# Kernel optimization log

Measured on AMD Instinct MI355X. Metric: run time of the kernel, lower is better.

The kernel has to match this reference:

```python
import jax, jax.numpy as jnp
import numpy as np

D_MODEL = 48
SSM_RATIO = 2
D_INNER = D_MODEL * SSM_RATIO   # 96
D_STATE = 16
DT_RANK = -(-D_MODEL // 16)     # ceil(48/16) = 3
K = 4                           # 4 scan directions
LAP_ITERS = 10
LAP_TAU = 0.1
B, DD, HH, WW = 2, 20, 20, 20   # L = 8000 (even)


def _lap_kernel(c):
    k = np.zeros((3, 3, 3), dtype=np.float32)
    k[1, 1, 1] = -6.0
    k[0, 1, 1] = k[2, 1, 1] = 1.0
    k[1, 0, 1] = k[1, 2, 1] = 1.0
    k[1, 1, 0] = k[1, 1, 2] = 1.0
    return jnp.asarray(np.tile(k[None, None], (c, 1, 1, 1, 1)))  # (C,1,3,3,3)


def _dwconv3d(x, w):
    # x: (B,C,D,H,W), w: (C,1,3,3,3) depthwise
    return jax.lax.conv_general_dilated(
        x, w, (1, 1, 1), 'SAME',
        dimension_numbers=('NCDHW', 'OIDHW', 'NCDHW'),
        feature_group_count=x.shape[1])


def _directions(feat):
    # feat: (B,C,D,H,W) -> (B,4,C,L): forward, flipped-L, channel-flipped, cross
    Bb, C, Dd, Hh, Ww = feat.shape
    L = Dd * Hh * Ww
    f = feat.reshape(Bb, C, L)
    bwd = f[:, :, ::-1]
    cb = feat[:, ::-1].reshape(Bb, C, L)
    half = (L + 1) // 2            # L is even here
    front = np.arange(half)
    back = np.arange(half, L)[::-1]
    cross_idx = np.stack([front, back], axis=1).reshape(-1)[:L]
    cross = f[:, :, cross_idx]
    return jnp.stack([f, bwd, cb, cross], axis=1)


def _selective_scan(u, delta, A, Bs, Cs, Ds):
    # u, delta: (b,k,d,l); A: (k,d,n); Bs, Cs: (b,k,n,l); Ds: (k,d)
    dl = jnp.moveaxis(delta, -1, 0)  # (l,b,k,d)
    ul = jnp.moveaxis(u, -1, 0)
    Bl = jnp.moveaxis(Bs, -1, 0)     # (l,b,k,n)
    Cl = jnp.moveaxis(Cs, -1, 0)
    h0 = jnp.zeros(u.shape[:3] + (A.shape[-1],), u.dtype)  # (b,k,d,n)

    def step(h, inp):
        d_t, u_t, b_t, c_t = inp
        dA = jnp.exp(d_t[..., None] * A[None])                    # (b,k,d,n)
        h = dA * h + (d_t * u_t)[..., None] * b_t[:, :, None, :]  # (b,k,d,n)
        y = jnp.einsum('bkdn,bkn->bkd', h, c_t)
        return h, y

    _, ys = jax.lax.scan(step, h0, (dl, ul, Bl, Cl))
    y = jnp.moveaxis(ys, 0, -1)  # (b,k,d,l)
    return y + Ds[None, :, :, None] * u


def setup_inputs() -> dict:
    key = jax.random.key(0)
    ks = jax.random.split(key, 10)

    def rn(k, shape, scale=0.02):
        return jax.random.normal(k, shape, dtype=jnp.float32) * scale

    x = jax.random.normal(ks[0], (B, DD, HH, WW, D_MODEL), dtype=jnp.float32)
    in_proj_w = rn(ks[1], (2 * D_INNER, D_MODEL))
    in_proj_cross_w = rn(ks[2], (D_INNER, D_MODEL))
    conv_w = rn(ks[3], (D_INNER, 1, 3, 3, 3), 0.1)
    conv_b = jnp.zeros((D_INNER,), jnp.float32)
    x_proj_weight = rn(ks[4], (K, DT_RANK + 2 * D_STATE, D_INNER))
    dt_std = DT_RANK ** -0.5
    dt_projs_weight = jax.random.uniform(ks[5], (K, D_INNER, DT_RANK), minval=-dt_std, maxval=dt_std, dtype=jnp.float32)
    dt = jnp.exp(jax.random.uniform(ks[6], (K, D_INNER)) * (np.log(0.1) - np.log(0.001)) + np.log(0.001))
    dt = jnp.clip(dt, 1e-4, None)
    dt_projs_bias = dt + jnp.log(-jnp.expm1(-dt))  # inverse softplus
    A_logs = jnp.log(jnp.tile(jnp.arange(1, D_STATE + 1, dtype=jnp.float32)[None], (K * D_INNER, 1)))
    Ds = jnp.ones((K * D_INNER,), jnp.float32)
    out_norm_w = jnp.ones((D_INNER,), jnp.float32)
    out_norm_b = jnp.zeros((D_INNER,), jnp.float32)
    out_proj_w = rn(ks[7], (D_MODEL, D_INNER))
    concat_w = rn(ks[8], (D_MODEL, 2 * D_MODEL))
    concat_b = jnp.zeros((D_MODEL,), jnp.float32)
    return dict(x=x, in_proj_w=in_proj_w, in_proj_cross_w=in_proj_cross_w,
                conv_w=conv_w, conv_b=conv_b, x_proj_weight=x_proj_weight,
                dt_projs_weight=dt_projs_weight, dt_projs_bias=dt_projs_bias,
                A_logs=A_logs, Ds=Ds, out_norm_w=out_norm_w, out_norm_b=out_norm_b,
                out_proj_w=out_proj_w, concat_w=concat_w, concat_b=concat_b)


def reference(x, in_proj_w, in_proj_cross_w, conv_w, conv_b, x_proj_weight,
              dt_projs_weight, dt_projs_bias, A_logs, Ds, out_norm_w,
              out_norm_b, out_proj_w, concat_w, concat_b):
    Bb, Dd, Hh, Ww, C = x.shape
    L = Dd * Hh * Ww
    xch = jnp.moveaxis(x, -1, 1)  # (B,C,D,H,W)

    # --- 3D Laplacian frequency decomposition: u_{k+1} = u_k + tau * lap(u_k)
    lap_k = _lap_kernel(C)
    u = xch
    for _ in range(LAP_ITERS):
        u = u + LAP_TAU * _dwconv3d(u, lap_k)
    low, high = u, xch - u
    cat = jnp.concatenate([low, high], axis=1)  # (B,2C,D,H,W)
    # 1x1x1 conv 2C -> C
    x_f = jnp.einsum('bcdhw,oc->bodhw', cat, concat_w) + concat_b[None, :, None, None, None]

    # --- CSS3D(x, x_f)
    xz = x @ in_proj_w.T                       # (B,D,H,W,2*d_inner)
    xi, z = jnp.split(xz, 2, axis=-1)
    xc = jnp.moveaxis(x_f, 1, -1) @ in_proj_cross_w.T  # (B,D,H,W,d_inner)
    xi = jnp.moveaxis(xi, -1, 1)               # (B,d_inner,D,H,W)
    xi = jax.nn.silu(_dwconv3d(xi, conv_w) + conv_b[None, :, None, None, None])
    xc = jnp.moveaxis(xc, -1, 1)

    xs = _directions(xi)    # (B,4,d_inner,L)
    xcs = _directions(xc)

    x_dbl = jnp.einsum('bkdl,kcd->bkcl', xcs, x_proj_weight)
    dts = x_dbl[:, :, :DT_RANK]
    Bs = x_dbl[:, :, DT_RANK:DT_RANK + D_STATE]
    Cs = x_dbl[:, :, DT_RANK + D_STATE:]
    dts = jnp.einsum('bkrl,kdr->bkdl', dts, dt_projs_weight)
    delta = jax.nn.softplus(dts + dt_projs_bias[None, :, :, None])
    A = -jnp.exp(A_logs.reshape(K, D_INNER, D_STATE))

    y = _selective_scan(xs, delta, A, Bs, Cs, Ds.reshape(K, D_INNER))
    y = y.mean(axis=1).reshape(Bb, D_INNER, Dd, Hh, Ww)
    y = jnp.moveaxis(y, 1, -1)                 # (B,D,H,W,d_inner)

    mu = y.mean(-1, keepdims=True)
    var = ((y - mu) ** 2).mean(-1, keepdims=True)
    y = (y - mu) / jnp.sqrt(var + 1e-5) * out_norm_w + out_norm_b

    y = y * jax.nn.sigmoid(z)
    return y @ out_proj_w.T                    # (B,D,H,W,d_model)
```

## Files before the change

kernel.cpp:

```cpp
#include <hip/hip_runtime.h>
#include <hip/hip_bf16.h>

typedef __hip_bfloat16 bf16;
typedef unsigned short u16;

#define L_  8000
#define CM  48
#define DI  96
#define DST 16
#define BB  2
#define NC  64
#define CS  125

#define W_IPW    0
#define W_IPCW   9216
#define W_CW     13824
#define W_CB     16416
#define W_XPW    16512
#define W_DTW    29952
#define W_DTB    31104
#define W_ALOG   31488
#define W_DSP    37632
#define W_NW     38016
#define W_NB     38112
#define W_OPW    38208
#define W_CCW    42816
#define W_CCB    47424
#define W_CVT_END 47472
#define W_WU     47472
#define W_WX     52080
#define W_BC     56688
#define W_ZT     56784
#define W_XIRAW  1592784
#define W_XT     3128784
#define W_UT     3896784
#define W_DTS    1592784
#define W_P      1784784
#define W_HLOC   2571216
#define W_HSTART 3357648
#define W_XIT    4664784
#define W_XCT    6200784
#define W_Y      4664784
#define W_F32_END 7736784
#define H_UP 0
#define H_BS 6144000
#define H_CS 7168000
#define H_END 8192000
#define NEED_BYTES ((size_t)W_F32_END*4 + (size_t)H_END*2)

__device__ __forceinline__ float b2f(bf16 v){ return __bfloat162float(v); }
__device__ __forceinline__ float bf2f(u16 v){ return __uint_as_float(((unsigned)v) << 16); }
__device__ __forceinline__ u16   f2b(float f){ bf16 h = __float2bfloat16(f); return *(u16*)&h; }
__device__ __forceinline__ float softplus(float tv){
    return fmaxf(tv, 0.f) + __logf(1.f + __expf(-fabsf(tv)));
}
template<int CTRL>
__device__ __forceinline__ float dppadd(float v){
    int x = __builtin_amdgcn_update_dpp(0, __float_as_int(v), CTRL, 0xF, 0xF, true);
    return v + __int_as_float(x);
}

__global__ __launch_bounds__(256) void k_xt(const void* __restrict__ xin,
                                            const u16* __restrict__ probe,
                                            float* __restrict__ xt){
    __shared__ float tileS[CM][65];
    int tile = blockIdx.x;
    int b = tile / 125, lt = (tile - b*125)*64;
    bool isb = (probe[0] != 0);
    for (int i = threadIdx.x; i < 64*CM; i += 256){
        int l = i / CM, c = i - (i/CM)*CM;
        size_t gi = ((size_t)b*L_ + lt + l)*CM + c;
        float v = isb ? b2f(((const bf16*)xin)[gi]) : ((const float*)xin)[gi];
        tileS[c][l] = v;
    }
    __syncthreads();
    for (int i = threadIdx.x; i < CM*64; i += 256){
        int c = i >> 6, l = i & 63;
        xt[((size_t)(b*CM + c))*L_ + lt + l] = tileS[c][l];
    }
}

struct CvtArgs { const void* src[15]; int beg[16]; };

__global__ __launch_bounds__(256) void k_cvt(CvtArgs a, float* __restrict__ dst){
    int i = blockIdx.x*256 + threadIdx.x;
    if (i >= W_CVT_END) return;
    bool isb = (((const u16*)a.src[9])[0] != 0);
    int s = 1;
    #pragma unroll
    for (int t = 2; t < 15; ++t) if (i >= a.beg[t]) s = t;
    int j = i - a.beg[s];
    dst[i] = isb ? b2f(((const bf16*)a.src[s])[j]) : ((const float*)a.src[s])[j];
}

__global__ __launch_bounds__(256) void k_zero_out(const u16* __restrict__ probe, void* out){
    int i = blockIdx.x*256 + threadIdx.x;
    if (i >= BB*L_*CM) return;
    if (probe[0] != 0) ((u16*)out)[i] = 0;
    else               ((unsigned*)out)[i] = 0;
}

__global__ __launch_bounds__(256) void k_prew(const float* __restrict__ ipcw,
                                              const float* __restrict__ ccw,
                                              const float* __restrict__ ccb,
                                              float* __restrict__ Wu, float* __restrict__ Wx,
                                              float* __restrict__ bc){
    int i = blockIdx.x*256 + threadIdx.x;
    if (i >= DI*CM) return;
    int j = i / CM, m = i - j*CM;
    float s1 = 0.f, s2 = 0.f;
    for (int o = 0; o < CM; ++o){
        float w = ipcw[j*CM + o];
        s1 = fmaf(w, ccw[o*DI + m],      s1);
        s2 = fmaf(w, ccw[o*DI + CM + m], s2);
    }
    Wx[i] = s2; Wu[i] = s1 - s2;
    if (m == 0){
        float sb = 0.f;
        for (int o = 0; o < CM; ++o) sb = fmaf(ipcw[j*CM + o], ccb[o], sb);
        bc[j] = sb;
    }
}

#define LSTR  24
#define LSLAB (22*LSTR)
__global__ __launch_bounds__(1024) void k_lap(const float* __restrict__ xt,
                                              float* __restrict__ ut){
    __shared__ float buf[2][22*LSLAB];
    int bc = blockIdx.x;
    for (int i = threadIdx.x; i < 2*22*LSLAB; i += 1024) ((float*)buf)[i] = 0.f;
    __syncthreads();
    const float* xp = xt + (size_t)bc*L_;
    for (int v = threadIdx.x; v < L_; v += 1024){
        int d = v/400, r = v - 400*d, h = r/20, w = r - 20*h;
        buf[0][(d+1)*LSLAB + (h+1)*LSTR + (w+2)] = xp[v];
    }
    __syncthreads();
    int cur = 0;
    for (int it = 0; it < 10; ++it){
        int nxt = cur ^ 1;
        const float* bcur = buf[cur];
        float* bnxt = buf[nxt];
        for (int tk = threadIdx.x; tk < 2000; tk += 1024){
            int d = tk/100; int rem = tk - 100*d; int h = rem/5; int w0 = (rem - 5*h)*4;
            int base = (d+1)*LSLAB + (h+1)*LSTR + (w0+2);
            float2 c01 = *(const float2*)&bcur[base];
            float2 c23 = *(const float2*)&bcur[base+2];
            float  eL  = bcur[base-1], eR = bcur[base+4];
            float2 u01 = *(const float2*)&bcur[base-LSTR],  u23 = *(const float2*)&bcur[base-LSTR+2];
            float2 d01 = *(const float2*)&bcur[base+LSTR],  d23 = *(const float2*)&bcur[base+LSTR+2];
            float2 m01 = *(const float2*)&bcur[base-LSLAB], m23 = *(const float2*)&bcur[base-LSLAB+2];
            float2 p01 = *(const float2*)&bcur[base+LSLAB], p23 = *(const float2*)&bcur[base+LSLAB+2];
            float s0 = eL    + c01.y + u01.x + d01.x + m01.x + p01.x;
            float s1 = c01.x + c23.x + u01.y + d01.y + m01.y + p01.y;
            float s2 = c01.y + c23.y + u23.x + d23.x + m23.x + p23.x;
            float s3 = c23.x + eR    + u23.y + d23.y + m23.y + p23.y;
            float2 r01, r23;
            r01.x = fmaf(0.1f, s0 - 6.f*c01.x, c01.x);
            r01.y = fmaf(0.1f, s1 - 6.f*c01.y, c01.y);
            r23.x = fmaf(0.1f, s2 - 6.f*c23.x, c23.x);
            r23.y = fmaf(0.1f, s3 - 6.f*c23.y, c23.y);
            *(float2*)&bnxt[base]   = r01;
            *(float2*)&bnxt[base+2] = r23;
        }
        __syncthreads();
        cur = nxt;
    }
    float* uo = ut + (size_t)bc*L_;
    for (int v = threadIdx.x; v < L_; v += 1024){
        int d = v/400, r = v - 400*d, h = r/20, w = r - 20*h;
        uo[v] = buf[cur][(d+1)*LSLAB + (h+1)*LSTR + (w+2)];
    }
}

__global__ __launch_bounds__(256) void k_proj_xz(const float* __restrict__ xt,
                                                 const float* __restrict__ ipw,
                                                 float* __restrict__ xi_raw,
                                                 float* __restrict__ zt){
    __shared__ float w[2*DI*CM];
    for (int i = threadIdx.x; i < 2*DI*CM; i += 256) w[i] = ipw[i];
    __syncthreads();
    int sub = threadIdx.x >> 6;
    int lane = threadIdx.x & 63;
    int v = blockIdx.x*64 + lane;
    int b = v / L_, l = v - b*L_;
    float xv[CM];
    #pragma unroll
    for (int c = 0; c < CM; ++c) xv[c] = xt[((size_t)(b*CM + c))*L_ + l];
    for (int jj = 0; jj < 48; ++jj){
        int j = sub*48 + jj;
        float s = 0.f;
        #pragma unroll
        for (int c = 0; c < CM; ++c) s = fmaf(w[j*CM + c], xv[c], s);
        if (sub < 2) xi_raw[((size_t)(b*DI + j))*L_ + l] = s;
        else         zt[((size_t)(b*DI + (j - DI)))*L_ + l] = s;
    }
}

__global__ __launch_bounds__(256) void k_proj_xc(const float* __restrict__ xt,
                                                 const float* __restrict__ ut,
                                                 const float* __restrict__ Wu,
                                                 const float* __restrict__ Wx,
                                                 const float* __restrict__ bc,
                                                 float* __restrict__ xct){
    __shared__ float wu_s[DI*CM], wx_s[DI*CM], bc_s[DI];
    for (int i = threadIdx.x; i < DI*CM; i += 256){ wu_s[i] = Wu[i]; wx_s[i] = Wx[i]; }
    if (threadIdx.x < DI) bc_s[threadIdx.x] = bc[threadIdx.x];
    __syncthreads();
    int sub = threadIdx.x >> 6;
    int lane = threadIdx.x & 63;
    int v = blockIdx.x*64 + lane;
    int b = v / L_, l = v - b*L_;
    float uv[CM], xv[CM];
    #pragma unroll
    for (int c = 0; c < CM; ++c){
        uv[c] = ut[((size_t)(b*CM + c))*L_ + l];
        xv[c] = xt[((size_t)(b*CM + c))*L_ + l];
    }
    for (int jj = 0; jj < 24; ++jj){
        int j = sub*24 + jj;
        float s = bc_s[j];
        #pragma unroll
        for (int m = 0; m < CM; ++m){
            s = fmaf(wu_s[j*CM + m], uv[m], s);
            s = fmaf(wx_s[j*CM + m], xv[m], s);
        }
        xct[((size_t)(b*DI + j))*L_ + l] = s;
    }
}

__global__ __launch_bounds__(512) void k_conv(const float* __restrict__ xi_raw,
                                              const float* __restrict__ cwv,
                                              const float* __restrict__ cbv,
                                              float* __restrict__ xit){
    __shared__ float in_s[L_];
    int bc = blockIdx.x;
    int b = bc / DI, c = bc - b*DI;
    const float* src = xi_raw + (size_t)bc*L_;
    for (int v = threadIdx.x; v < L_; v += 512) in_s[v] = src[v];
    float w[27];
    #pragma unroll
    for (int i = 0; i < 27; ++i) w[i] = cwv[c*27 + i];
    float bias = cbv[c];
    __syncthreads();
    float* dst = xit + (size_t)bc*L_;
    for (int v = threadIdx.x; v < L_; v += 512){
        int d = v / 400; int r = v - d*400; int h = r / 20; int ww = r - h*20;
        float s = bias;
        #pragma unroll
        for (int kd = 0; kd < 3; ++kd){
            int dd = d + kd - 1; if (dd < 0 || dd > 19) continue;
            #pragma unroll
            for (int kh = 0; kh < 3; ++kh){
                int hh = h + kh - 1; if (hh < 0 || hh > 19) continue;
                #pragma unroll
                for (int kw = 0; kw < 3; ++kw){
                    int wv = ww + kw - 1; if (wv < 0 || wv > 19) continue;
                    s = fmaf(w[kd*9+kh*3+kw], in_s[(dd*20+hh)*20+wv], s);
                }
            }
        }
        float sig = 1.f / (1.f + __expf(-s));
        dst[v] = s * sig;
    }
}

__global__ __launch_bounds__(256) void k_xdbl(const float* __restrict__ xct,
                                              const float* __restrict__ xit,
                                              const float* __restrict__ xpw,
                                              float* __restrict__ dts,
                                              u16* __restrict__ up,
                                              u16* __restrict__ Bso,
                                              u16* __restrict__ Cso){
    __shared__ float xpw_s[35*DI];
    int bk = blockIdx.y;
    int b = bk >> 2, k = bk & 3;
    for (int i = threadIdx.x; i < 35*DI; i += 256) xpw_s[i] = xpw[(size_t)k*35*DI + i];
    __syncthreads();
    int l = blockIdx.x*256 + threadIdx.x;
    if (l >= L_) return;
    int ls;
    if (k == 1)      ls = L_-1-l;
    else if (k == 3) ls = (l & 1) ? (L_-1-(l>>1)) : (l>>1);
    else             ls = l;
    bool flip = (k == 2);
    float acc[35];
    #pragma unroll
    for (int c = 0; c < 35; ++c) acc[c] = 0.f;
    for (int dd = 0; dd < DI; ++dd){
        float v = xct[((size_t)(b*DI + (flip ? DI-1-dd : dd)))*L_ + ls];
        #pragma unroll
        for (int c = 0; c < 35; ++c) acc[c] = fmaf(v, xpw_s[c*DI + dd], acc[c]);
    }
    size_t bcbase = ((size_t)bk*DST)*L_ + l;
    #pragma unroll
    for (int n = 0; n < DST; ++n){
        Bso[bcbase + (size_t)n*L_] = f2b(acc[3+n]);
        Cso[bcbase + (size_t)n*L_] = f2b(acc[19+n]);
    }
    size_t dtsbase = ((size_t)bk*3)*L_ + l;
    #pragma unroll
    for (int r = 0; r < 3; ++r) dts[dtsbase + (size_t)r*L_] = acc[r];
    const float* xib = xit + (size_t)b*DI*L_;
    size_t ub = (size_t)bk*DI*L_ + l;
    for (int dd = 0; dd < DI; ++dd){
        int dp = flip ? (DI-1-dd) : dd;
        up[ub + (size_t)dd*L_] = f2b(xib[(size_t)dp*L_ + ls]);
    }
}

#define SCAN_LDS 24096
template<int PASS>
__global__ __launch_bounds__(192) void k_scan(const float* __restrict__ dts,
                                              const float* __restrict__ dtw,
                                              const float* __restrict__ dtb,
                                              const float* __restrict__ alog,
                                              const float* __restrict__ dsp,
                                              const u16* __restrict__ up,
                                              const u16* __restrict__ bs_g,
                                              const u16* __restrict__ cs_g,
                                              const float* __restrict__ hstart,
                                              float* __restrict__ P,
                                              float* __restrict__ Hloc,
                                              u16* __restrict__ y_g){
    extern __shared__ char smem[];
    float* dts4 = (float*)smem;
    u16*   bc_s = (u16*)(smem + 2000);
    u16*   u_s  = (u16*)(smem + 12000);

    int chunk = blockIdx.x, bk = blockIdx.y, dg = blockIdx.z;
    int t = threadIdx.x, k = bk & 3;
    size_t dtsbase = (size_t)bk*3*L_ + (size_t)chunk*CS;
    for (int i = t; i < CS; i += 192){
        float4 v;
        v.x = dts[dtsbase + i];
        v.y = dts[dtsbase + L_ + i];
        v.z = dts[dtsbase + 2*L_ + i];
        v.w = 0.f;
        *(float4*)&dts4[i*4] = v;
    }
    size_t bcb = ((size_t)bk*DST)*L_ + (size_t)chunk*CS;
    for (int i = t; i < DST*CS; i += 192){
        int n = i/CS, col = i - n*CS;
        bc_s[col*40 + n] = bs_g[bcb + (size_t)n*L_ + col];
        if (PASS == 3) bc_s[col*40 + 16 + n] = cs_g[bcb + (size_t)n*L_ + col];
    }
    size_t upb = ((size_t)bk*DI + dg*48)*L_ + (size_t)chunk*CS;
    for (int i = t; i < 48*CS; i += 192){
        int dl = i/CS, col = i - dl*CS;
        u_s[dl*126 + col] = up[upb + (size_t)dl*L_ + col];
    }
    int dloc = t >> 2, nq = t & 3, d = dg*48 + dloc;
    int gd = k*DI + d;
    float w0 = dtw[gd*3], w1 = dtw[gd*3+1], w2 = dtw[gd*3+2], bia = dtb[gd];
    float a2[4];
    #pragma unroll
    for (int j = 0; j < 4; ++j)
        a2[j] = -__expf(alog[gd*DST + nq*4 + j]) * 1.44269504f;
    float dsD = dsp[gd];
    float h[4];
    if (PASS == 1){
        #pragma unroll
        for (int j = 0; j < 4; ++j) h[j] = 0.f;
    } else {
        float4 hv = *(const float4*)&hstart[(((size_t)(bk*NC + chunk))*DI + d)*DST + nq*4];
        h[0] = hv.x; h[1] = hv.y; h[2] = hv.z; h[3] = hv.w;
    }
    float S = 0.f;
    __syncthreads();

    const u16* ur = u_s + dloc*126;
    u16* yrow = y_g + ((size_t)bk*L_ + (size_t)chunk*CS)*DI + d;

    for (int l = 0; l < CS; ++l){
        float4 dt4 = *(const float4*)&dts4[l*4];
        float tv = fmaf(dt4.x, w0, fmaf(dt4.y, w1, fmaf(dt4.z, w2, bia)));
        float ds = softplus(tv);
        float uu = bf2f(ur[l]);
        float dsu = ds * uu;
        ushort4 bv = *(const ushort4*)&bc_s[l*40 + nq*4];
        float e[4];
        #pragma unroll
        for (int j = 0; j < 4; ++j) e[j] = __builtin_amdgcn_exp2f(ds * a2[j]);
        h[0] = fmaf(e[0], h[0], dsu * bf2f(bv.x));
        h[1] = fmaf(e[1], h[1], dsu * bf2f(bv.y));
        h[2] = fmaf(e[2], h[2], dsu * bf2f(bv.z));
        h[3] = fmaf(e[3], h[3], dsu * bf2f(bv.w));
        if (PASS == 1){
            S += ds;
        } else {
            ushort4 cv = *(const ushort4*)&bc_s[l*40 + 16 + nq*4];
            float y = h[0]*bf2f(cv.x);
            y = fmaf(h[1], bf2f(cv.y), y);
            y = fmaf(h[2], bf2f(cv.z), y);
            y = fmaf(h[3], bf2f(cv.w), y);
            y = dppadd<0xB1>(y);
            y = dppadd<0x4E>(y);
            if (nq == 0) yrow[(size_t)l*DI] = f2b(fmaf(dsD, uu, y));
        }
    }
    if (PASS == 1){
        size_t idx = (((size_t)(bk*NC + chunk))*DI + d)*DST + nq*4;
        float4 pv, hv;
        pv.x = __builtin_amdgcn_exp2f(S*a2[0]); pv.y = __builtin_amdgcn_exp2f(S*a2[1]);
        pv.z = __builtin_amdgcn_exp2f(S*a2[2]); pv.w = __builtin_amdgcn_exp2f(S*a2[3]);
        hv.x = h[0]; hv.y = h[1]; hv.z = h[2]; hv.w = h[3];
        *(float4*)&P[idx] = pv;
        *(float4*)&Hloc[idx] = hv;
    }
}

__global__ __launch_bounds__(256) void k_scan_mid(const float* __restrict__ P,
                                                  const float* __restrict__ Hloc,
                                                  float* __restrict__ Hstart){
    int blk = blockIdx.x;
    int bk = blk / 6, s = blk - bk*6;
    int t = threadIdx.x;
    size_t base = (size_t)bk*NC*DI*DST + s*256 + t;
    float h = 0.f;
    float pq[4], lq[4];
    #pragma unroll
    for (int j = 0; j < 4; ++j){ pq[j] = P[base + (size_t)j*1536]; lq[j] = Hloc[base + (size_t)j*1536]; }
    for (int c = 0; c < NC; ++c){
        float pn = 0.f, ln = 0.f;
        if (c + 4 < NC){
            pn = P[base + (size_t)(c+4)*1536];
            ln = Hloc[base + (size_t)(c+4)*1536];
        }
        size_t cb = base + (size_t)c*1536;
        Hstart[cb] = h;
        int r = c & 3;
        h = fmaf(pq[r], h, lq[r]);
        pq[r] = pn; lq[r] = ln;
    }
}

__global__ __launch_bounds__(256) void k_final(const u16* __restrict__ y,
                                               const float* __restrict__ zt,
                                               const float* __restrict__ nw,
                                               const float* __restrict__ nb,
                                               const float* __restrict__ opw,
                                               const u16* __restrict__ probe,
                                               void* __restrict__ out){
    __shared__ float opw_s[CM*100];
    __shared__ float ynorm[32*100];
    __shared__ float nw_s[DI], nb_s[DI];
    __shared__ u16   ostage[32*CM];
    for (int i = threadIdx.x; i < CM*DI; i += 256){
        int o = i / DI, dd = i - o*DI;
        opw_s[o*100 + dd] = opw[i];
    }
    if (threadIdx.x < DI){ nw_s[threadIdx.x] = nw[threadIdx.x]; nb_s[threadIdx.x] = nb[threadIdx.x]; }
    __syncthreads();
    int t = threadIdx.x, sub = t & 7, vi = t >> 3;
    int v = blockIdx.x*32 + vi;
    int b = v / L_, l = v - b*L_;
    int dd0 = sub*12;
    float yv[12];
    #pragma unroll
    for (int j = 0; j < 12; ++j) yv[j] = 0.f;
    #pragma unroll
    for (int k = 0; k < 4; ++k){
        const u16* yp = y + (((size_t)(b*4 + k))*L_ + l)*DI + dd0;
        ushort4 aa = *(const ushort4*)yp;
        ushort4 bb = *(const ushort4*)(yp + 4);
        ushort4 cc = *(const ushort4*)(yp + 8);
        yv[0] += bf2f(aa.x); yv[1] += bf2f(aa.y); yv[2]  += bf2f(aa.z); yv[3]  += bf2f(aa.w);
        yv[4] += bf2f(bb.x); yv[5] += bf2f(bb.y); yv[6]  += bf2f(bb.z); yv[7]  += bf2f(bb.w);
        yv[8] += bf2f(cc.x); yv[9] += bf2f(cc.y); yv[10] += bf2f(cc.z); yv[11] += bf2f(cc.w);
    }
    float mu = 0.f;
    #pragma unroll
    for (int j = 0; j < 12; ++j){ yv[j] *= 0.25f; mu += yv[j]; }
    mu += __shfl_xor(mu, 1); mu += __shfl_xor(mu, 2); mu += __shfl_xor(mu, 4);
    mu *= (1.f/DI);
    float var = 0.f;
    #pragma unroll
    for (int j = 0; j < 12; ++j){ float tv = yv[j] - mu; var = fmaf(tv, tv, var); }
    var += __shfl_xor(var, 1); var += __shfl_xor(var, 2); var += __shfl_xor(var, 4);
    var *= (1.f/DI);
    float rstd = rsqrtf(var + 1e-5f);
    #pragma unroll
    for (int j = 0; j < 12; ++j){
        int dd = dd0 + j;
        float g = fmaf((yv[j] - mu)*rstd, nw_s[dd], nb_s[dd]);
        float zz = zt[((size_t)(b*DI + dd))*L_ + l];
        ynorm[vi*100 + dd] = g / (1.f + __expf(-zz));
    }
    __syncthreads();
    bool isb = (probe[0] != 0);
    #pragma unroll
    for (int oi = 0; oi < 6; ++oi){
        int o = sub*6 + oi;
        float s = 0.f;
        #pragma unroll
        for (int c = 0; c < 24; ++c){
            float4 yy = *(const float4*)&ynorm[vi*100 + c*4];
            float4 ww = *(const float4*)&opw_s[o*100 + c*4];
            s = fmaf(yy.x, ww.x, s); s = fmaf(yy.y, ww.y, s);
            s = fmaf(yy.z, ww.z, s); s = fmaf(yy.w, ww.w, s);
        }
        if (isb) ostage[vi*CM + o] = f2b(s);
        else     ((float*)out)[(size_t)v*CM + o] = s;
    }
    __syncthreads();
    if (isb){
        u16* orow = (u16*)out + (size_t)blockIdx.x*32*CM;
        for (int i = threadIdx.x; i < 32*CM; i += 256) orow[i] = ostage[i];
    }
}

extern "C" void kernel_launch(void* const* d_in, const int* in_sizes, int n_in,
                              void* d_out, int out_size, void* d_ws, size_t ws_size,
                              hipStream_t stream) {
    const u16* probe = (const u16*)d_in[9];

    if (ws_size < NEED_BYTES){
        k_zero_out<<<(BB*L_*CM + 255)/256, 256, 0, stream>>>(probe, d_out);
        return;
    }

    float* F  = (float*)d_ws;
    u16*  Hb  = (u16*)((char*)d_ws + (size_t)W_F32_END*4);
    u16*  up  = Hb + H_UP;
    u16*  bs  = Hb + H_BS;
    u16*  cs  = Hb + H_CS;
    u16*  yb  = (u16*)(F + W_Y);

    CvtArgs a;
    static const int beg[16] = {-1, W_IPW, W_IPCW, W_CW, W_CB, W_XPW, W_DTW, W_DTB,
                                W_ALOG, W_DSP, W_NW, W_NB, W_OPW, W_CCW, W_CCB, W_CVT_END};
    for (int i = 0; i < 15; ++i) a.src[i] = d_in[i];
    for (int i = 0; i < 16; ++i) a.beg[i] = beg[i];

    k_xt     <<<250, 256, 0, stream>>>(d_in[0], probe, F + W_XT);
    k_cvt    <<<(W_CVT_END + 255)/256, 256, 0, stream>>>(a, F);
    k_prew   <<<(DI*CM + 255)/256, 256, 0, stream>>>(F + W_IPCW, F + W_CCW, F + W_CCB,
                                                     F + W_WU, F + W_WX, F + W_BC);
    k_lap    <<<BB*CM, 1024, 0, stream>>>(F + W_XT, F + W_UT);
    k_proj_xz<<<250, 256, 0, stream>>>(F + W_XT, F + W_IPW, F + W_XIRAW, F + W_ZT);
    k_proj_xc<<<250, 256, 0, stream>>>(F + W_XT, F + W_UT, F + W_WU, F + W_WX, F + W_BC, F + W_XCT);
    k_conv   <<<BB*DI, 512, 0, stream>>>(F + W_XIRAW, F + W_CW, F + W_CB, F + W_XIT);
    k_xdbl   <<<dim3(32, BB*4), 256, 0, stream>>>(F + W_XCT, F + W_XIT, F + W_XPW,
                                                  F + W_DTS, up, bs, cs);
    k_scan<1><<<dim3(NC, BB*4, 2), 192, SCAN_LDS, stream>>>(F + W_DTS, F + W_DTW, F + W_DTB,
                                                            F + W_ALOG, F + W_DSP, up, bs, cs,
                                                            F + W_HSTART, F + W_P, F + W_HLOC, yb);
    k_scan_mid<<<BB*4*6, 256, 0, stream>>>(F + W_P, F + W_HLOC, F + W_HSTART);
    k_scan<3><<<dim3(NC, BB*4, 2), 192, SCAN_LDS, stream>>>(F + W_DTS, F + W_DTW, F + W_DTB,
                                                            F + W_ALOG, F + W_DSP, up, bs, cs,
                                                            F + W_HSTART, F + W_P, F + W_HLOC, yb);
    k_final  <<<500, 256, 0, stream>>>(yb, F + W_ZT, F + W_NW, F + W_NB, F + W_OPW, probe, d_out);
}
```

Baseline: 394.6 us.

## Split projection kernels across output halves and tile xdbl through shared memory

Measured after the change: 348.3 us. 1.13x faster.

```diff
diff --git a/kernel.cpp b/kernel.cpp
--- a/kernel.cpp
+++ b/kernel.cpp
@@ -59,6 +59,11 @@
     int x = __builtin_amdgcn_update_dpp(0, __float_as_int(v), CTRL, 0xF, 0xF, true);
     return v + __int_as_float(x);
 }
+__device__ __forceinline__ int lperm(int k, int gl){
+    if (k == 1) return L_-1-gl;
+    if (k == 3) return (gl & 1) ? (L_-1-(gl>>1)) : (gl>>1);
+    return gl;
+}
 
 __global__ __launch_bounds__(256) void k_xt(const void* __restrict__ xin,
                                             const u16* __restrict__ probe,
@@ -177,8 +182,9 @@
                                                  const float* __restrict__ ipw,
                                                  float* __restrict__ xi_raw,
                                                  float* __restrict__ zt){
-    __shared__ float w[2*DI*CM];
-    for (int i = threadIdx.x; i < 2*DI*CM; i += 256) w[i] = ipw[i];
+    __shared__ float w[DI*CM];
+    int jh = blockIdx.y;
+    for (int i = threadIdx.x; i < DI*CM; i += 256) w[i] = ipw[jh*DI*CM + i];
     __syncthreads();
     int sub = threadIdx.x >> 6;
     int lane = threadIdx.x & 63;
@@ -187,13 +193,13 @@
     float xv[CM];
     #pragma unroll
     for (int c = 0; c < CM; ++c) xv[c] = xt[((size_t)(b*CM + c))*L_ + l];
-    for (int jj = 0; jj < 48; ++jj){
-        int j = sub*48 + jj;
+    float* dst = (jh == 0) ? xi_raw : zt;
+    for (int jj = 0; jj < 24; ++jj){
+        int j = sub*24 + jj;
         float s = 0.f;
         #pragma unroll
         for (int c = 0; c < CM; ++c) s = fmaf(w[j*CM + c], xv[c], s);
-        if (sub < 2) xi_raw[((size_t)(b*DI + j))*L_ + l] = s;
-        else         zt[((size_t)(b*DI + (j - DI)))*L_ + l] = s;
+        dst[((size_t)(b*DI + j))*L_ + l] = s;
     }
 }
 
@@ -203,9 +209,13 @@
                                                  const float* __restrict__ Wx,
                                                  const float* __restrict__ bc,
                                                  float* __restrict__ xct){
-    __shared__ float wu_s[DI*CM], wx_s[DI*CM], bc_s[DI];
-    for (int i = threadIdx.x; i < DI*CM; i += 256){ wu_s[i] = Wu[i]; wx_s[i] = Wx[i]; }
-    if (threadIdx.x < DI) bc_s[threadIdx.x] = bc[threadIdx.x];
+    __shared__ float wu_s[48*CM], wx_s[48*CM], bc_s[48];
+    int jh = blockIdx.y;
+    for (int i = threadIdx.x; i < 48*CM; i += 256){
+        wu_s[i] = Wu[jh*48*CM + i];
+        wx_s[i] = Wx[jh*48*CM + i];
+    }
+    if (threadIdx.x < 48) bc_s[threadIdx.x] = bc[jh*48 + threadIdx.x];
     __syncthreads();
     int sub = threadIdx.x >> 6;
     int lane = threadIdx.x & 63;
@@ -217,15 +227,15 @@
         uv[c] = ut[((size_t)(b*CM + c))*L_ + l];
         xv[c] = xt[((size_t)(b*CM + c))*L_ + l];
     }
-    for (int jj = 0; jj < 24; ++jj){
-        int j = sub*24 + jj;
-        float s = bc_s[j];
+    for (int jj = 0; jj < 12; ++jj){
+        int jl = sub*12 + jj;
+        float s = bc_s[jl];
         #pragma unroll
         for (int m = 0; m < CM; ++m){
-            s = fmaf(wu_s[j*CM + m], uv[m], s);
-            s = fmaf(wx_s[j*CM + m], xv[m], s);
-        }
-        xct[((size_t)(b*DI + j))*L_ + l] = s;
+            s = fmaf(wu_s[jl*CM + m], uv[m], s);
+            s = fmaf(wx_s[jl*CM + m], xv[m], s);
+        }
+        xct[((size_t)(b*DI + jh*48 + jl))*L_ + l] = s;
     }
 }
 
@@ -272,40 +282,44 @@
                                               u16* __restrict__ up,
                                               u16* __restrict__ Bso,
                                               u16* __restrict__ Cso){
-    __shared__ float xpw_s[35*DI];
-    int bk = blockIdx.y;
-    int b = bk >> 2, k = bk & 3;
-    for (int i = threadIdx.x; i < 35*DI; i += 256) xpw_s[i] = xpw[(size_t)k*35*DI + i];
-    __syncthreads();
-    int l = blockIdx.x*256 + threadIdx.x;
-    if (l >= L_) return;
-    int ls;
-    if (k == 1)      ls = L_-1-l;
-    else if (k == 3) ls = (l & 1) ? (L_-1-(l>>1)) : (l>>1);
-    else             ls = l;
+    __shared__ float xpw_s[36*DI];
+    __shared__ float xct_s[DI*64];
+    int bk = blockIdx.y, b = bk >> 2, k = bk & 3;
+    int lt = blockIdx.x*64;
+    int t = threadIdx.x;
     bool flip = (k == 2);
-    float acc[35];
-    #pragma unroll
-    for (int c = 0; c < 35; ++c) acc[c] = 0.f;
-    for (int dd = 0; dd < DI; ++dd){
-        float v = xct[((size_t)(b*DI + (flip ? DI-1-dd : dd)))*L_ + ls];
-        #pragma unroll
-        for (int c = 0; c < 35; ++c) acc[c] = fmaf(v, xpw_s[c*DI + dd], acc[c]);
-    }
-    size_t bcbase = ((size_t)bk*DST)*L_ + l;
-    #pragma unroll
-    for (int n = 0; n < DST; ++n){
-        Bso[bcbase + (size_t)n*L_] = f2b(acc[3+n]);
-        Cso[bcbase + (size_t)n*L_] = f2b(acc[19+n]);
-    }
-    size_t dtsbase = ((size_t)bk*3)*L_ + l;
-    #pragma unroll
-    for (int r = 0; r < 3; ++r) dts[dtsbase + (size_t)r*L_] = acc[r];
-    const float* xib = xit + (size_t)b*DI*L_;
-    size_t ub = (size_t)bk*DI*L_ + l;
-    for (int dd = 0; dd < DI; ++dd){
+    for (int i = t; i < 36*DI; i += 256) xpw_s[i] = (i < 35*DI) ? xpw[(size_t)k*35*DI + i] : 0.f;
+    for (int i = t; i < DI*64; i += 256){
+        int dd = i >> 6, l = i & 63;
+        int ls = lperm(k, lt + l);
         int dp = flip ? (DI-1-dd) : dd;
-        up[ub + (size_t)dd*L_] = f2b(xib[(size_t)dp*L_ + ls]);
+        xct_s[((dd >> 2)*64 + l)*4 + (dd & 3)] = xct[((size_t)(b*DI + dp))*L_ + ls];
+    }
+    __syncthreads();
+    int sub = t >> 6, l = t & 63, gl = lt + l;
+    float acc[9];
+    #pragma unroll
+    for (int j = 0; j < 9; ++j) acc[j] = 0.f;
+    for (int dd4 = 0; dd4 < 24; ++dd4){
+        float4 v = *(const float4*)&xct_s[(dd4*64 + l)*4];
+        #pragma unroll
+        for (int j = 0; j < 9; ++j){
+            float4 w = *(const float4*)&xpw_s[(sub*9 + j)*DI + dd4*4];
+            acc[j] = fmaf(v.x, w.x, fmaf(v.y, w.y, fmaf(v.z, w.z, fmaf(v.w, w.w, acc[j]))));
+        }
+    }
+    #pragma unroll
+    for (int j = 0; j < 9; ++j){
+        int c = sub*9 + j;
+        if (c < 3)       dts[((size_t)bk*3 + c)*L_ + gl] = acc[j];
+        else if (c < 19) Bso[((size_t)bk*DST + (c-3))*L_ + gl]  = f2b(acc[j]);
+        else if (c < 35) Cso[((size_t)bk*DST + (c-19))*L_ + gl] = f2b(acc[j]);
+    }
+    for (int i = t; i < DI*64; i += 256){
+        int dd = i >> 6, l2 = i & 63;
+        int ls = lperm(k, lt + l2);
+        int dp = flip ? (DI-1-dd) : dd;
+        up[((size_t)bk*DI + dd)*L_ + lt + l2] = f2b(xit[((size_t)(b*DI + dp))*L_ + ls]);
     }
 }
 
@@ -418,18 +432,18 @@
     int t = threadIdx.x;
     size_t base = (size_t)bk*NC*DI*DST + s*256 + t;
     float h = 0.f;
-    float pq[4], lq[4];
-    #pragma unroll
-    for (int j = 0; j < 4; ++j){ pq[j] = P[base + (size_t)j*1536]; lq[j] = Hloc[base + (size_t)j*1536]; }
+    float pq[8], lq[8];
+    #pragma unroll
+    for (int j = 0; j < 8; ++j){ pq[j] = P[base + (size_t)j*1536]; lq[j] = Hloc[base + (size_t)j*1536]; }
     for (int c = 0; c < NC; ++c){
         float pn = 0.f, ln = 0.f;
-        if (c + 4 < NC){
-            pn = P[base + (size_t)(c+4)*1536];
-            ln = Hloc[base + (size_t)(c+4)*1536];
+        if (c + 8 < NC){
+            pn = P[base + (size_t)(c+8)*1536];
+            ln = Hloc[base + (size_t)(c+8)*1536];
         }
         size_t cb = base + (size_t)c*1536;
         Hstart[cb] = h;
-        int r = c & 3;
+        int r = c & 7;
         h = fmaf(pq[r], h, lq[r]);
         pq[r] = pn; lq[r] = ln;
     }
@@ -538,11 +552,11 @@
     k_prew   <<<(DI*CM + 255)/256, 256, 0, stream>>>(F + W_IPCW, F + W_CCW, F + W_CCB,
                                                      F + W_WU, F + W_WX, F + W_BC);
     k_lap    <<<BB*CM, 1024, 0, stream>>>(F + W_XT, F + W_UT);
-    k_proj_xz<<<250, 256, 0, stream>>>(F + W_XT, F + W_IPW, F + W_XIRAW, F + W_ZT);
-    k_proj_xc<<<250, 256, 0, stream>>>(F + W_XT, F + W_UT, F + W_WU, F + W_WX, F + W_BC, F + W_XCT);
+    k_proj_xz<<<dim3(250,2), 256, 0, stream>>>(F + W_XT, F + W_IPW, F + W_XIRAW, F + W_ZT);
+    k_proj_xc<<<dim3(250,2), 256, 0, stream>>>(F + W_XT, F + W_UT, F + W_WU, F + W_WX, F + W_BC, F + W_XCT);
     k_conv   <<<BB*DI, 512, 0, stream>>>(F + W_XIRAW, F + W_CW, F + W_CB, F + W_XIT);
-    k_xdbl   <<<dim3(32, BB*4), 256, 0, stream>>>(F + W_XCT, F + W_XIT, F + W_XPW,
-                                                  F + W_DTS, up, bs, cs);
+    k_xdbl   <<<dim3(125, BB*4), 256, 0, stream>>>(F + W_XCT, F + W_XIT, F + W_XPW,
+                                                   F + W_DTS, up, bs, cs);
     k_scan<1><<<dim3(NC, BB*4, 2), 192, SCAN_LDS, stream>>>(F + W_DTS, F + W_DTW, F + W_DTB,
                                                             F + W_ALOG, F + W_DSP, up, bs, cs,
                                                             F + W_HSTART, F + W_P, F + W_HLOC, yb);
```
